# Kernel tuning notes

Measured on AMD Instinct MI355X. Metric: run time of the kernel, lower is better.

## Reference

```python
import jax, jax.numpy as jnp
import numpy as np

B, S, D_MODEL, N_HEADS = 2, 2048, 1024, 16
HEAD_DIM = D_MODEL // N_HEADS
BASE = 10000.0

# 3D RoPE slice sizes: n_pairs = head_dim//2 split into x,y,z
_n_pairs = HEAD_DIM // 2
_px = _n_pairs // 3
_py = _n_pairs // 3
_pz = _n_pairs - _px - _py
D_X, D_Y, D_Z = _px * 2, _py * 2, _pz * 2  # 20, 20, 24


def _rotate_half(x):
    # interleaved pairs: (x0,x1,x2,x3,...) -> (-x1,x0,-x3,x2,...)
    x1 = x[..., ::2]
    x2 = x[..., 1::2]
    return jnp.stack((-x2, x1), axis=-1).reshape(x.shape)


def _rope_apply(x, pos, dim):
    # x: [B,H,S,dim]; pos: [B,S] int coords
    if dim == 0:
        return x
    inv_freq = 1.0 / (BASE ** (jnp.arange(0, dim, 2, dtype=jnp.float32) / dim))
    t = pos.astype(jnp.float32)[..., None] * inv_freq          # [B,S,dim//2]
    cos = jnp.repeat(jnp.cos(t), 2, axis=-1)[:, None]          # [B,1,S,dim]
    sin = jnp.repeat(jnp.sin(t), 2, axis=-1)[:, None]
    return x * cos + _rotate_half(x) * sin


def _rope3d(q, k, pos_xyz):
    s1, s2, s3 = D_X, D_X + D_Y, D_X + D_Y + D_Z
    parts_q, parts_k = [], []
    for (a, b), ax in (((0, s1), 0), ((s1, s2), 1), ((s2, s3), 2)):
        d = b - a
        parts_q.append(_rope_apply(q[..., a:b], pos_xyz[..., ax], d))
        parts_k.append(_rope_apply(k[..., a:b], pos_xyz[..., ax], d))
    return jnp.concatenate(parts_q, axis=-1), jnp.concatenate(parts_k, axis=-1)


def setup_inputs() -> dict:
    key = jax.random.key(0)
    k1, k2, k3, k4 = jax.random.split(key, 4)
    hidden_states = jax.random.normal(k1, (B, S, D_MODEL), dtype=jnp.float32)
    # padding: each batch row keeps first `len` tokens
    lengths = jnp.array([S - 37, S - 130], dtype=jnp.int32)
    attention_mask = jnp.arange(S)[None, :] < lengths[:, None]          # [B,S] bool, True=keep
    causal_mask = jnp.triu(jnp.ones((S, S), dtype=bool), k=1)[None, None]  # True=masked
    pos_xyz = jax.random.randint(k2, (B, S, 3), 0, 30).astype(jnp.int32)
    w_qkv = jax.random.normal(k3, (3 * D_MODEL, D_MODEL), dtype=jnp.float32) * (D_MODEL ** -0.5)
    w_out = jax.random.normal(k4, (D_MODEL, D_MODEL), dtype=jnp.float32) * (D_MODEL ** -0.5)
    return {"hidden_states": hidden_states, "w_qkv": w_qkv, "w_out": w_out,
            "attention_mask": attention_mask, "causal_mask": causal_mask,
            "pos_xyz": pos_xyz}


def reference(hidden_states, w_qkv, w_out, attention_mask, causal_mask, pos_xyz):
    Bb, Ss, Dd = hidden_states.shape
    scale = HEAD_DIM ** -0.5
    qkv = jnp.einsum('bsd,ed->bse', hidden_states, w_qkv)               # [B,S,3D]
    qkv = qkv.reshape(Bb, Ss, 3, N_HEADS, HEAD_DIM).transpose(2, 0, 3, 1, 4)
    q, k, v = qkv[0], qkv[1], qkv[2]                                    # [B,H,S,hd]
    q, k = _rope3d(q, k, pos_xyz)
    scores = jnp.einsum('bhqd,bhkd->bhqk', q, k) * scale                # [B,H,S,S]
    scores = jnp.where(causal_mask, -jnp.inf, scores)
    scores = jnp.where(attention_mask[:, None, None, :], scores, -jnp.inf)
    weights = jax.nn.softmax(scores, axis=-1)                           # dropout p=0 (eval)
    out = jnp.einsum('bhqk,bhkd->bhqd', weights, v)
    out = out.transpose(0, 2, 1, 3).reshape(Bb, Ss, Dd)
    return jnp.einsum('bsd,ed->bse', out, w_out)
```

## Files before the change

### kernel.cpp

```cpp
#include <hip/hip_runtime.h>
#include <math.h>

extern "C" __device__ float __ocml_native_exp2_f32(float);

namespace {

typedef __attribute__((ext_vector_type(8))) short short8;
typedef __attribute__((ext_vector_type(4))) short short4b;
typedef __attribute__((ext_vector_type(4))) float floatx4;

constexpr int B_ = 2;
constexpr int S_ = 2048;
constexpr int DM_ = 1024;
constexpr int NH_ = 16;
constexpr int HD_ = 64;

__device__ inline unsigned short f2bf(float f) {
  unsigned u = __builtin_bit_cast(unsigned, f);
  u += 0x7fffu + ((u >> 16) & 1u);
  return (unsigned short)(u >> 16);
}

template <int CTRL>
__device__ inline float dpp_ror(float x) {
  const int r = __builtin_amdgcn_update_dpp(
      0, __builtin_bit_cast(int, x), CTRL, 0xF, 0xF, false);
  return __builtin_bit_cast(float, r);
}

__device__ inline void gl2lds16(const unsigned short* g, unsigned short* l) {
  __builtin_amdgcn_global_load_lds(
      (const __attribute__((address_space(1))) unsigned int*)g,
      (__attribute__((address_space(3))) unsigned int*)l, 16, 0, 0);
}

__global__ void cvt_bf16(const float* __restrict__ in,
                         unsigned short* __restrict__ out, int n8) {
  const int i = blockIdx.x * blockDim.x + threadIdx.x;
  if (i >= n8) return;
  const float4 a = ((const float4*)in)[i * 2];
  const float4 b = ((const float4*)in)[i * 2 + 1];
  short8 v;
  v[0] = (short)f2bf(a.x); v[1] = (short)f2bf(a.y);
  v[2] = (short)f2bf(a.z); v[3] = (short)f2bf(a.w);
  v[4] = (short)f2bf(b.x); v[5] = (short)f2bf(b.y);
  v[6] = (short)f2bf(b.z); v[7] = (short)f2bf(b.w);
  ((short8*)out)[i] = v;
}

__global__ void lengths_kernel(const unsigned char* __restrict__ mask,
                               int* __restrict__ lengths) {
  const int es1 = (mask[1] != 0);
  const int b = blockIdx.x;
  __shared__ int cnt;
  if (threadIdx.x == 0) cnt = 0;
  __syncthreads();
  int local = 0;
  for (int s = threadIdx.x; s < S_; s += blockDim.x) {
    bool nz;
    if (es1) nz = mask[b * S_ + s] != 0;
    else     nz = ((const unsigned int*)mask)[b * S_ + s] != 0;
    local += nz ? 1 : 0;
  }
  atomicAdd(&cnt, local);
  __syncthreads();
  if (threadIdx.x == 0) lengths[b] = cnt;
}

__global__ __launch_bounds__(256) void qkv_gemm(
    const unsigned short* __restrict__ A, const unsigned short* __restrict__ W,
    const int* __restrict__ pos_xyz,
    unsigned short* __restrict__ Qb, unsigned short* __restrict__ Kb,
    unsigned short* __restrict__ Vtb) {
  __shared__ __align__(16) unsigned short As[128 * 32];
  __shared__ __align__(16) unsigned short Bs[128 * 32];
  const int m0 = blockIdx.y * 128, n0 = blockIdx.x * 128;
  const int w = threadIdx.x >> 6, lane = threadIdx.x & 63;
  const int lm = lane & 15, q4 = lane >> 4;
  const int srow = w * 32;
  const int r_in = lane >> 2, c_in = (lane & 3) * 8;
  const int wr = (w >> 1) * 64, wc = (w & 1) * 64;
  const int which = n0 >> 10;
  floatx4 acc[4][4];
  const floatx4 z4 = {0.f, 0.f, 0.f, 0.f};
#pragma unroll
  for (int i = 0; i < 4; i++)
#pragma unroll
    for (int j = 0; j < 4; j++) acc[i][j] = z4;

  for (int k0 = 0; k0 < DM_; k0 += 32) {
    gl2lds16(A + (size_t)(m0 + srow + r_in) * DM_ + k0 + c_in, As + srow * 32);
    gl2lds16(A + (size_t)(m0 + srow + 16 + r_in) * DM_ + k0 + c_in,
             As + (srow + 16) * 32);
    gl2lds16(W + (size_t)(n0 + srow + r_in) * DM_ + k0 + c_in, Bs + srow * 32);
    gl2lds16(W + (size_t)(n0 + srow + 16 + r_in) * DM_ + k0 + c_in,
             Bs + (srow + 16) * 32);
    __syncthreads();
    short8 af[4], bf[4];
#pragma unroll
    for (int t = 0; t < 4; t++)
      af[t] = *(const short8*)(As + (wr + t * 16 + lm) * 32 + q4 * 8);
#pragma unroll
    for (int t = 0; t < 4; t++)
      bf[t] = *(const short8*)(Bs + (wc + t * 16 + lm) * 32 + q4 * 8);
    if (which == 2) {
#pragma unroll
      for (int i = 0; i < 4; i++)
#pragma unroll
        for (int j = 0; j < 4; j++)
          acc[i][j] = __builtin_amdgcn_mfma_f32_16x16x32_bf16(af[i], bf[j],
                                                              acc[i][j], 0, 0, 0);
    } else {
#pragma unroll
      for (int i = 0; i < 4; i++)
#pragma unroll
        for (int j = 0; j < 4; j++)
          acc[i][j] = __builtin_amdgcn_mfma_f32_16x16x32_bf16(bf[i], af[j],
                                                              acc[i][j], 0, 0, 0);
    }
    __syncthreads();
  }

  const int h = ((n0 + wc) & 1023) >> 6;
  if (which == 2) {
#pragma unroll
    for (int nt = 0; nt < 4; nt++) {
      const int d = nt * 16 + lm;
#pragma unroll
      for (int mt = 0; mt < 4; mt++) {
        const int m = m0 + wr + mt * 16 + q4 * 4;
        const int bi = m >> 11, si = m & (S_ - 1);
        short4b pk;
#pragma unroll
        for (int r = 0; r < 4; r++) pk[r] = (short)f2bf(acc[mt][nt][r]);
        *(short4b*)(Vtb + ((size_t)(bi * NH_ + h) * HD_ + d) * S_ + si) = pk;
      }
    }
  } else {
    unsigned short* Dst = (which == 0) ? Qb : Kb;
    const float osc = (which == 0) ? 0.125f * 1.44269504088896f : 1.0f;
#pragma unroll
    for (int nt = 0; nt < 4; nt++) {
      const int dbase = nt * 16 + q4 * 4;
      const int p0 = dbase >> 1;
      int axis, j0, dseg;
      if (p0 < 10)      { axis = 0; j0 = p0;      dseg = 20; }
      else if (p0 < 20) { axis = 1; j0 = p0 - 10; dseg = 20; }
      else              { axis = 2; j0 = p0 - 20; dseg = 24; }
      const float invf0 =
          __expf(-(2.0f * (float)j0 / (float)dseg) * 9.210340371976184f);
      const float invf1 =
          __expf(-(2.0f * (float)(j0 + 1) / (float)dseg) * 9.210340371976184f);
#pragma unroll
      for (int mt = 0; mt < 4; mt++) {
        const int m = m0 + wr + mt * 16 + lm;
        const int bi = m >> 11, si = m & (S_ - 1);
        const int pos = pos_xyz[((size_t)bi * S_ + si) * 3 + axis];
        short4b pk;
#pragma unroll
        for (int u = 0; u < 2; u++) {
          const float ve = acc[nt][mt][2 * u], vo = acc[nt][mt][2 * u + 1];
          float sn, cs;
          sincosf((float)pos * (u ? invf1 : invf0), &sn, &cs);
          pk[2 * u]     = (short)f2bf(fmaf(ve, cs, -vo * sn) * osc);
          pk[2 * u + 1] = (short)f2bf(fmaf(vo, cs, ve * sn) * osc);
        }
        *(short4b*)(Dst + ((size_t)(bi * NH_ + h) * S_ + si) * HD_ + dbase) = pk;
      }
    }
  }
}

__global__ __launch_bounds__(256) void flash_mfma(
    const unsigned short* __restrict__ Q, const unsigned short* __restrict__ Kg,
    const unsigned short* __restrict__ Vt, const int* __restrict__ lengths,
    unsigned short* __restrict__ Oa) {
  __shared__ __align__(16) unsigned short Ks[2 * 64 * 64];
  __shared__ __align__(16) unsigned short Vs[2 * 64 * 64];
  __shared__ __align__(16) unsigned short Ps[4][16 * 64];

  const int lin = blockIdx.y * gridDim.x + blockIdx.x;
  const int xcd = lin & 7, k = lin >> 3;
  const int s = k >> 5, c = k & 31;
  const int pc = (c & 1) ? 31 - (c >> 1) : (c >> 1);
  const int qt = (s & 1) ? 31 - pc : pc;
  const int bh = xcd * 4 + s;
  const int b = bh >> 4, h = bh & 15;
  const int q0 = qt * 64;

  const int w = threadIdx.x >> 6, lane = threadIdx.x & 63;
  const int lm = lane & 15, q4 = lane >> 4;
  const int len = lengths[b];
  const unsigned short* Qp = Q + (size_t)bh * S_ * HD_;
  const unsigned short* Kp = Kg + (size_t)bh * S_ * HD_;
  const unsigned short* Vp = Vt + (size_t)bh * HD_ * S_;

  const int r8 = lane >> 3, c8 = lane & 7;
  const int rs0 = w * 16 + r8, rs1 = rs0 + 8;
  const int cs = (c8 ^ (rs0 & 7)) << 3;
  const unsigned short* gK0 = Kp + (size_t)rs0 * HD_ + cs;
  const unsigned short* gK1 = Kp + (size_t)rs1 * HD_ + cs;
  const unsigned short* gV0 = Vp + (size_t)rs0 * S_ + cs;
  const unsigned short* gV1 = Vp + (size_t)rs1 * S_ + cs;
  unsigned short* dK0 = Ks + w * 16 * 64;
  unsigned short* dK1 = Ks + (w * 16 + 8) * 64;
  unsigned short* dV0 = Vs + w * 16 * 64;
  unsigned short* dV1 = Vs + (w * 16 + 8) * 64;

  const int qrow = q0 + w * 16 + lm;
  short8 qf[2];
  qf[0] = *(const short8*)(Qp + (size_t)qrow * HD_ + q4 * 8);
  qf[1] = *(const short8*)(Qp + (size_t)qrow * HD_ + 32 + q4 * 8);

  const floatx4 z4 = {0.f, 0.f, 0.f, 0.f};
  floatx4 o[4];
#pragma unroll
  for (int dt = 0; dt < 4; dt++) o[dt] = z4;
  float m_i[4], l_i[4];
#pragma unroll
  for (int r = 0; r < 4; r++) { m_i[r] = -1e30f; l_i[r] = 0.0f; }

  unsigned short* ps = Ps[w];
  const int ktiles = min(qt + 1, (len + 63) >> 6);

  gl2lds16(gK0, dK0);
  gl2lds16(gK1, dK1);
  gl2lds16(gV0, dV0);
  gl2lds16(gV1, dV1);
  __syncthreads();

  int cur = 0;
  for (int kt = 0; kt < ktiles; kt++) {
    const int k0 = kt * 64;
    if (kt + 1 < ktiles) {
      const size_t koff = (size_t)(k0 + 64) * HD_;
      const int nb = (cur ^ 1) * 4096;
      gl2lds16(gK0 + koff, dK0 + nb);
      gl2lds16(gK1 + koff, dK1 + nb);
      gl2lds16(gV0 + (k0 + 64), dV0 + nb);
      gl2lds16(gV1 + (k0 + 64), dV1 + nb);
    }
    const unsigned short* kc = Ks + cur * 4096;
    const unsigned short* vc = Vs + cur * 4096;

    floatx4 sc[4];
#pragma unroll
    for (int nt = 0; nt < 4; nt++) {
      const int row = nt * 16 + lm, sw = row & 7;
      const unsigned short* kb = kc + row * 64;
      const short8 b0 = *(const short8*)(kb + ((q4 ^ sw) << 3));
      const short8 b1 = *(const short8*)(kb + (((q4 + 4) ^ sw) << 3));
      sc[nt] = __builtin_amdgcn_mfma_f32_16x16x32_bf16(qf[0], b0, z4, 0, 0, 0);
      sc[nt] = __builtin_amdgcn_mfma_f32_16x16x32_bf16(qf[1], b1, sc[nt], 0, 0, 0);
    }
    if (kt == qt || k0 + 64 > len) {
#pragma unroll
      for (int nt = 0; nt < 4; nt++) {
        const int col = k0 + nt * 16 + lm;
#pragma unroll
        for (int r = 0; r < 4; r++) {
          const int row = q0 + w * 16 + q4 * 4 + r;
          if (col > row || col >= len) sc[nt][r] = -1e30f;
        }
      }
    }
#pragma unroll
    for (int r = 0; r < 4; r++) {
      float mx = fmaxf(fmaxf(sc[0][r], sc[1][r]), fmaxf(sc[2][r], sc[3][r]));
      mx = fmaxf(mx, dpp_ror<0x121>(mx));
      mx = fmaxf(mx, dpp_ror<0x122>(mx));
      mx = fmaxf(mx, dpp_ror<0x124>(mx));
      mx = fmaxf(mx, dpp_ror<0x128>(mx));
      const float mt = fmaxf(m_i[r], mx);
      const float al = __ocml_native_exp2_f32(m_i[r] - mt);
      float rs = 0.0f;
#pragma unroll
      for (int nt = 0; nt < 4; nt++) {
        const float pp = __ocml_native_exp2_f32(sc[nt][r] - mt);
        sc[nt][r] = pp;
        rs += pp;
      }
      rs += dpp_ror<0x121>(rs);
      rs += dpp_ror<0x122>(rs);
      rs += dpp_ror<0x124>(rs);
      rs += dpp_ror<0x128>(rs);
      l_i[r] = l_i[r] * al + rs;
      m_i[r] = mt;
#pragma unroll
      for (int dt = 0; dt < 4; dt++) o[dt][r] *= al;
    }
#pragma unroll
    for (int nt = 0; nt < 4; nt++)
#pragma unroll
      for (int r = 0; r < 4; r++) {
        const int row = q4 * 4 + r;
        const int cc = (((nt * 2 + (lm >> 3)) ^ (row & 7)) << 3) | (lm & 7);
        ps[row * 64 + cc] = f2bf(sc[nt][r]);
      }
#pragma unroll
    for (int ks = 0; ks < 2; ks++) {
      const short8 pf = *(const short8*)(
          ps + lm * 64 + ((((ks << 2) + q4) ^ (lm & 7)) << 3));
#pragma unroll
      for (int dt = 0; dt < 4; dt++) {
        const int row = dt * 16 + lm, sw = row & 7;
        const short8 vf = *(const short8*)(
            vc + row * 64 + ((((ks << 2) + q4) ^ sw) << 3));
        o[dt] = __builtin_amdgcn_mfma_f32_16x16x32_bf16(pf, vf, o[dt], 0, 0, 0);
      }
    }
    __syncthreads();
    cur ^= 1;
  }
  float invl[4];
#pragma unroll
  for (int r = 0; r < 4; r++) invl[r] = 1.0f / l_i[r];
#pragma unroll
  for (int dt = 0; dt < 4; dt++)
#pragma unroll
    for (int r = 0; r < 4; r++) {
      const int row = q0 + w * 16 + q4 * 4 + r;
      const int col = h * HD_ + dt * 16 + lm;
      Oa[((size_t)b * S_ + row) * DM_ + col] = f2bf(o[dt][r] * invl[r]);
    }
}

__global__ __launch_bounds__(256) void out_gemm(
    const unsigned short* __restrict__ A, const unsigned short* __restrict__ W,
    float* __restrict__ C) {
  __shared__ __align__(16) unsigned short As[128 * 32];
  __shared__ __align__(16) unsigned short Bs[128 * 32];
  const int m0 = blockIdx.y * 128, n0 = blockIdx.x * 128;
  const int w = threadIdx.x >> 6, lane = threadIdx.x & 63;
  const int lm = lane & 15, q4 = lane >> 4;
  const int srow = w * 32;
  const int r_in = lane >> 2, c_in = (lane & 3) * 8;
  const int wr = (w >> 1) * 64, wc = (w & 1) * 64;
  floatx4 acc[4][4];
  const floatx4 z4 = {0.f, 0.f, 0.f, 0.f};
#pragma unroll
  for (int i = 0; i < 4; i++)
#pragma unroll
    for (int j = 0; j < 4; j++) acc[i][j] = z4;

  for (int k0 = 0; k0 < DM_; k0 += 32) {
    gl2lds16(A + (size_t)(m0 + srow + r_in) * DM_ + k0 + c_in, As + srow * 32);
    gl2lds16(A + (size_t)(m0 + srow + 16 + r_in) * DM_ + k0 + c_in,
             As + (srow + 16) * 32);
    gl2lds16(W + (size_t)(n0 + srow + r_in) * DM_ + k0 + c_in, Bs + srow * 32);
    gl2lds16(W + (size_t)(n0 + srow + 16 + r_in) * DM_ + k0 + c_in,
             Bs + (srow + 16) * 32);
    __syncthreads();
    short8 af[4], bf[4];
#pragma unroll
    for (int t = 0; t < 4; t++)
      af[t] = *(const short8*)(As + (wr + t * 16 + lm) * 32 + q4 * 8);
#pragma unroll
    for (int t = 0; t < 4; t++)
      bf[t] = *(const short8*)(Bs + (wc + t * 16 + lm) * 32 + q4 * 8);
#pragma unroll
    for (int i = 0; i < 4; i++)
#pragma unroll
      for (int j = 0; j < 4; j++)
        acc[i][j] =
            __builtin_amdgcn_mfma_f32_16x16x32_bf16(bf[i], af[j], acc[i][j],
                                                    0, 0, 0);
    __syncthreads();
  }
#pragma unroll
  for (int nt = 0; nt < 4; nt++) {
    const int nbase = n0 + wc + nt * 16 + q4 * 4;
#pragma unroll
    for (int mt = 0; mt < 4; mt++) {
      const int m = m0 + wr + mt * 16 + lm;
      *(floatx4*)(C + (size_t)m * DM_ + nbase) = acc[nt][mt];
    }
  }
}

}

extern "C" void kernel_launch(void* const* d_in, const int* in_sizes, int n_in,
                              void* d_out, int out_size, void* d_ws, size_t ws_size,
                              hipStream_t stream) {
  const float* hidden = (const float*)d_in[0];
  const float* w_qkv = (const float*)d_in[1];
  const float* w_out = (const float*)d_in[2];
  const unsigned char* amask = (const unsigned char*)d_in[3];
  const int* pos_xyz = (const int*)d_in[5];
  float* out = (float*)d_out;

  constexpr size_t NHID = (size_t)B_ * S_ * DM_;
  constexpr size_t NWQ = (size_t)3 * DM_ * DM_;
  constexpr size_t NWO = (size_t)DM_ * DM_;
  constexpr size_t NQKV = (size_t)B_ * NH_ * S_ * HD_;

  unsigned short* hb = (unsigned short*)d_ws;
  unsigned short* wqb = hb + NHID;
  unsigned short* wob = wqb + NWQ;
  unsigned short* Qb = wob + NWO;
  unsigned short* Kb = Qb + NQKV;
  unsigned short* Vtb = Kb + NQKV;
  unsigned short* attn = Vtb + NQKV;
  int* lens = (int*)(attn + NQKV);

  cvt_bf16<<<dim3(NHID / 8 / 256), dim3(256), 0, stream>>>(hidden, hb,
                                                           (int)(NHID / 8));
  cvt_bf16<<<dim3(NWQ / 8 / 256), dim3(256), 0, stream>>>(w_qkv, wqb,
                                                          (int)(NWQ / 8));
  cvt_bf16<<<dim3(NWO / 8 / 256), dim3(256), 0, stream>>>(w_out, wob,
                                                          (int)(NWO / 8));
  lengths_kernel<<<dim3(B_), dim3(256), 0, stream>>>(amask, lens);
  qkv_gemm<<<dim3(3 * DM_ / 128, B_ * S_ / 128), dim3(256), 0, stream>>>(
      hb, wqb, pos_xyz, Qb, Kb, Vtb);
  flash_mfma<<<dim3(S_ / 64, B_ * NH_), dim3(256), 0, stream>>>(
      Qb, Kb, Vtb, lens, attn);
  out_gemm<<<dim3(DM_ / 128, B_ * S_ / 128), dim3(256), 0, stream>>>(
      attn, wob, out);
}
```

Baseline: 246.1 us.

## Fuse prep kernels, add MFMA priority hints, and lazily rescale softmax

Merges the three bf16 conversion kernels and the mask-length kernel into one launch to cut launch overhead. In the attention loop, raises wave priority around the MFMA blocks with s_setprio. It also skips the online-softmax rescale of the output and running sum unless some row's new max exceeds the old by more than 8. That lets probabilities reach up to 2^8 before rescaling, which risks slightly larger bf16 rounding in P.

New measurement: 240.5 us. -2.3%, faster.

```diff
diff --git a/kernel.cpp b/kernel.cpp
--- a/kernel.cpp
+++ b/kernel.cpp
@@ -34,37 +34,44 @@
       (__attribute__((address_space(3))) unsigned int*)l, 16, 0, 0);
 }
 
-__global__ void cvt_bf16(const float* __restrict__ in,
-                         unsigned short* __restrict__ out, int n8) {
-  const int i = blockIdx.x * blockDim.x + threadIdx.x;
-  if (i >= n8) return;
-  const float4 a = ((const float4*)in)[i * 2];
-  const float4 b = ((const float4*)in)[i * 2 + 1];
-  short8 v;
-  v[0] = (short)f2bf(a.x); v[1] = (short)f2bf(a.y);
-  v[2] = (short)f2bf(a.z); v[3] = (short)f2bf(a.w);
-  v[4] = (short)f2bf(b.x); v[5] = (short)f2bf(b.y);
-  v[6] = (short)f2bf(b.z); v[7] = (short)f2bf(b.w);
-  ((short8*)out)[i] = v;
-}
-
-__global__ void lengths_kernel(const unsigned char* __restrict__ mask,
-                               int* __restrict__ lengths) {
-  const int es1 = (mask[1] != 0);
-  const int b = blockIdx.x;
-  __shared__ int cnt;
-  if (threadIdx.x == 0) cnt = 0;
-  __syncthreads();
-  int local = 0;
-  for (int s = threadIdx.x; s < S_; s += blockDim.x) {
-    bool nz;
-    if (es1) nz = mask[b * S_ + s] != 0;
-    else     nz = ((const unsigned int*)mask)[b * S_ + s] != 0;
-    local += nz ? 1 : 0;
-  }
-  atomicAdd(&cnt, local);
-  __syncthreads();
-  if (threadIdx.x == 0) lengths[b] = cnt;
+__global__ __launch_bounds__(256) void prep(
+    const float* __restrict__ hidden, const float* __restrict__ wqkv,
+    const float* __restrict__ wout, const unsigned char* __restrict__ mask,
+    unsigned short* __restrict__ hb, int* __restrict__ lengths) {
+  const int bid = blockIdx.x;
+  if (bid < 4096) {
+    const int i = bid * 256 + threadIdx.x;
+    const float* src;
+    int off;
+    if (i < 524288)              { src = hidden; off = 0; }
+    else if (i < 524288 + 393216){ src = wqkv;   off = 524288; }
+    else                         { src = wout;   off = 524288 + 393216; }
+    const size_t j = (size_t)(i - off);
+    const float4 a = ((const float4*)src)[j * 2];
+    const float4 b = ((const float4*)src)[j * 2 + 1];
+    short8 v;
+    v[0] = (short)f2bf(a.x); v[1] = (short)f2bf(a.y);
+    v[2] = (short)f2bf(a.z); v[3] = (short)f2bf(a.w);
+    v[4] = (short)f2bf(b.x); v[5] = (short)f2bf(b.y);
+    v[6] = (short)f2bf(b.z); v[7] = (short)f2bf(b.w);
+    ((short8*)hb)[i] = v;
+  } else {
+    const int b = bid - 4096;
+    const int es1 = (mask[1] != 0);
+    __shared__ int cnt;
+    if (threadIdx.x == 0) cnt = 0;
+    __syncthreads();
+    int local = 0;
+    for (int s = threadIdx.x; s < S_; s += blockDim.x) {
+      bool nz;
+      if (es1) nz = mask[b * S_ + s] != 0;
+      else     nz = ((const unsigned int*)mask)[b * S_ + s] != 0;
+      local += nz ? 1 : 0;
+    }
+    atomicAdd(&cnt, local);
+    __syncthreads();
+    if (threadIdx.x == 0) lengths[b] = cnt;
+  }
 }
 
 __global__ __launch_bounds__(256) void qkv_gemm(
@@ -244,6 +251,7 @@
     const unsigned short* vc = Vs + cur * 4096;
 
     floatx4 sc[4];
+    __builtin_amdgcn_s_setprio(1);
 #pragma unroll
     for (int nt = 0; nt < 4; nt++) {
       const int row = nt * 16 + lm, sw = row & 7;
@@ -253,6 +261,7 @@
       sc[nt] = __builtin_amdgcn_mfma_f32_16x16x32_bf16(qf[0], b0, z4, 0, 0, 0);
       sc[nt] = __builtin_amdgcn_mfma_f32_16x16x32_bf16(qf[1], b1, sc[nt], 0, 0, 0);
     }
+    __builtin_amdgcn_s_setprio(0);
     if (kt == qt || k0 + 64 > len) {
 #pragma unroll
       for (int nt = 0; nt < 4; nt++) {
@@ -264,19 +273,35 @@
         }
       }
     }
+    float mx[4];
 #pragma unroll
     for (int r = 0; r < 4; r++) {
-      float mx = fmaxf(fmaxf(sc[0][r], sc[1][r]), fmaxf(sc[2][r], sc[3][r]));
-      mx = fmaxf(mx, dpp_ror<0x121>(mx));
-      mx = fmaxf(mx, dpp_ror<0x122>(mx));
-      mx = fmaxf(mx, dpp_ror<0x124>(mx));
-      mx = fmaxf(mx, dpp_ror<0x128>(mx));
-      const float mt = fmaxf(m_i[r], mx);
-      const float al = __ocml_native_exp2_f32(m_i[r] - mt);
+      float m0 = fmaxf(fmaxf(sc[0][r], sc[1][r]), fmaxf(sc[2][r], sc[3][r]));
+      m0 = fmaxf(m0, dpp_ror<0x121>(m0));
+      m0 = fmaxf(m0, dpp_ror<0x122>(m0));
+      m0 = fmaxf(m0, dpp_ror<0x124>(m0));
+      m0 = fmaxf(m0, dpp_ror<0x128>(m0));
+      mx[r] = m0;
+    }
+    const bool ok = (mx[0] <= m_i[0] + 8.f) && (mx[1] <= m_i[1] + 8.f) &&
+                    (mx[2] <= m_i[2] + 8.f) && (mx[3] <= m_i[3] + 8.f);
+    if (!__all(ok)) {
+#pragma unroll
+      for (int r = 0; r < 4; r++) {
+        const float mt = fmaxf(m_i[r], mx[r]);
+        const float al = __ocml_native_exp2_f32(m_i[r] - mt);
+        l_i[r] *= al;
+        m_i[r] = mt;
+#pragma unroll
+        for (int dt = 0; dt < 4; dt++) o[dt][r] *= al;
+      }
+    }
+#pragma unroll
+    for (int r = 0; r < 4; r++) {
       float rs = 0.0f;
 #pragma unroll
       for (int nt = 0; nt < 4; nt++) {
-        const float pp = __ocml_native_exp2_f32(sc[nt][r] - mt);
+        const float pp = __ocml_native_exp2_f32(sc[nt][r] - m_i[r]);
         sc[nt][r] = pp;
         rs += pp;
       }
@@ -284,10 +309,7 @@
       rs += dpp_ror<0x122>(rs);
       rs += dpp_ror<0x124>(rs);
       rs += dpp_ror<0x128>(rs);
-      l_i[r] = l_i[r] * al + rs;
-      m_i[r] = mt;
-#pragma unroll
-      for (int dt = 0; dt < 4; dt++) o[dt][r] *= al;
+      l_i[r] += rs;
     }
 #pragma unroll
     for (int nt = 0; nt < 4; nt++)
@@ -297,6 +319,7 @@
         const int cc = (((nt * 2 + (lm >> 3)) ^ (row & 7)) << 3) | (lm & 7);
         ps[row * 64 + cc] = f2bf(sc[nt][r]);
       }
+    __builtin_amdgcn_s_setprio(1);
 #pragma unroll
     for (int ks = 0; ks < 2; ks++) {
       const short8 pf = *(const short8*)(
@@ -309,6 +332,7 @@
         o[dt] = __builtin_amdgcn_mfma_f32_16x16x32_bf16(pf, vf, o[dt], 0, 0, 0);
       }
     }
+    __builtin_amdgcn_s_setprio(0);
     __syncthreads();
     cur ^= 1;
   }
@@ -404,13 +428,8 @@
   unsigned short* attn = Vtb + NQKV;
   int* lens = (int*)(attn + NQKV);
 
-  cvt_bf16<<<dim3(NHID / 8 / 256), dim3(256), 0, stream>>>(hidden, hb,
-                                                           (int)(NHID / 8));
-  cvt_bf16<<<dim3(NWQ / 8 / 256), dim3(256), 0, stream>>>(w_qkv, wqb,
-                                                          (int)(NWQ / 8));
-  cvt_bf16<<<dim3(NWO / 8 / 256), dim3(256), 0, stream>>>(w_out, wob,
-                                                          (int)(NWO / 8));
-  lengths_kernel<<<dim3(B_), dim3(256), 0, stream>>>(amask, lens);
+  prep<<<dim3(4096 + B_), dim3(256), 0, stream>>>(hidden, w_qkv, w_out, amask,
+                                                  hb, lens);
   qkv_gemm<<<dim3(3 * DM_ / 128, B_ * S_ / 128), dim3(256), 0, stream>>>(
       hb, wqb, pos_xyz, Qb, Kb, Vtb);
   flash_mfma<<<dim3(S_ / 64, B_ * NH_), dim3(256), 0, stream>>>(
```
